# Performance work log

Hardware: AMD Instinct MI355X
Metric: run time of the kernel (lower is better)

Reference implementation:

```python
import jax, jax.numpy as jnp
import numpy as np

EMBED = 1024
HEADS = 16
HEAD_DIM = EMBED // HEADS


def setup_inputs() -> dict:
    key = jax.random.key(0)
    ks = jax.random.split(key, 11)
    B, S, D = 2, 2048, EMBED
    scale = 1.0 / np.sqrt(D)
    inp = {
        "q": jax.random.normal(ks[0], (B, S, D), jnp.float32),
        "k": jax.random.normal(ks[1], (B, S, D), jnp.float32),
        "v": jax.random.normal(ks[2], (B, S, D), jnp.float32),
        "Wq": jax.random.normal(ks[3], (D, D), jnp.float32) * scale,
        "bq": jnp.zeros((D,), jnp.float32),
        "Wk": jax.random.normal(ks[4], (D, D), jnp.float32) * scale,
        "bk": jnp.zeros((D,), jnp.float32),
        "Wv": jax.random.normal(ks[5], (D, D), jnp.float32) * scale,
        "bv": jnp.zeros((D,), jnp.float32),
        "Wo": jax.random.normal(ks[6], (D, D), jnp.float32) * scale,
        "bo": jnp.zeros((D,), jnp.float32),
    }
    return inp


def _split_heads(x):
    b, n, c = x.shape
    return x.reshape(b, n, HEADS, c // HEADS).transpose(0, 2, 1, 3)  # [b,h,n,dh]


def reference(q, k, v, Wq, bq, Wk, bk, Wv, bv, Wo, bo):
    qh = _split_heads(q @ Wq + bq)
    kh = _split_heads(k @ Wk + bk)
    vh = _split_heads(v @ Wv + bv)
    scale = 1.0 / jnp.sqrt(jnp.asarray(HEAD_DIM, qh.dtype))
    att = jnp.einsum("bhqd,bhkd->bhqk", qh, kh) * scale
    att = jax.nn.softmax(att, axis=-1)
    out = jnp.einsum("bhqk,bhkd->bhqd", att, vh)
    b, h, n, dh = out.shape
    out = out.transpose(0, 2, 1, 3).reshape(b, n, h * dh)
    return out @ Wo + bo
```

## Files before the change

kernel.cpp:

```cpp
#include <hip/hip_runtime.h>
#include <hip/hip_bf16.h>
#include <stdint.h>

typedef unsigned short u16;
typedef __bf16 bf16x8 __attribute__((ext_vector_type(8)));
typedef float f32x4 __attribute__((ext_vector_type(4)));
typedef float f32x16 __attribute__((ext_vector_type(16)));
typedef unsigned int u32x4 __attribute__((ext_vector_type(4)));
typedef unsigned int u32x2 __attribute__((ext_vector_type(2)));

#define S_LEN 2048
#define DMODEL 1024
#define NHEAD 16
#define DHEAD 64
#define MROWS 4096
#define EXP2SCALE 0.180336880112f

__device__ __forceinline__ u16 f2b(float f) {
  __hip_bfloat16 h = __float2bfloat16(f);
  union { __hip_bfloat16 h; u16 u; } c;
  c.h = h;
  return c.u;
}
__device__ __forceinline__ unsigned int pk2(float lo, float hi) {
  return (unsigned int)f2b(lo) | ((unsigned int)f2b(hi) << 16);
}
__device__ __forceinline__ unsigned int cvtpk(float a, float b) {
  unsigned int r;
  asm("v_cvt_pk_bf16_f32 %0, %1, %2" : "=v"(r) : "v"(a), "v"(b));
  return r;
}
__device__ __forceinline__ void plswap(unsigned int &a, unsigned int &b) {
  auto r = __builtin_amdgcn_permlane32_swap((int)a, (int)b, false, false);
  a = (unsigned int)r[0];
  b = (unsigned int)r[1];
}

__device__ __forceinline__ void gload16(const void* g, void* l) {
  __builtin_amdgcn_global_load_lds(
      (const __attribute__((address_space(1))) unsigned int*)(uintptr_t)g,
      (__attribute__((address_space(3))) unsigned int*)(uintptr_t)l,
      16, 0, 0);
}

__global__ __launch_bounds__(256) void prep(
    const float* __restrict__ q, const float* __restrict__ k, const float* __restrict__ v,
    const float* __restrict__ Wq, const float* __restrict__ Wk,
    const float* __restrict__ Wv, const float* __restrict__ Wo,
    u16* __restrict__ Qx, u16* __restrict__ Kx, u16* __restrict__ Vx,
    u16* __restrict__ Wqt, u16* __restrict__ Wkt,
    u16* __restrict__ Wvt, u16* __restrict__ Wot) {
  __shared__ u16 tile[64][65];
  const int z = blockIdx.z;
  const int tid = threadIdx.x;
  if (z < 3) {
    const float* src = (z == 0) ? q : (z == 1) ? k : v;
    u16* dst = (z == 0) ? Qx : (z == 1) ? Kx : Vx;
    const size_t i8 = ((size_t)blockIdx.x * 256 + tid) * 8;
    float4 a = *(const float4*)(src + i8);
    float4 b = *(const float4*)(src + i8 + 4);
    u16 o[8];
    o[0] = f2b(a.x); o[1] = f2b(a.y); o[2] = f2b(a.z); o[3] = f2b(a.w);
    o[4] = f2b(b.x); o[5] = f2b(b.y); o[6] = f2b(b.z); o[7] = f2b(b.w);
    *(u32x4*)(dst + i8) = *(const u32x4*)o;
    return;
  }
  if (blockIdx.x >= 256) return;
  const int zz = z - 3;
  const float* W = (zz == 0) ? Wq : (zz == 1) ? Wk : (zz == 2) ? Wv : Wo;
  u16* Wt = (zz == 0) ? Wqt : (zz == 1) ? Wkt : (zz == 2) ? Wvt : Wot;
  const int n0 = (blockIdx.x & 15) * 64, k0 = (blockIdx.x >> 4) * 64;
#pragma unroll
  for (int j = 0; j < 16; j++) {
    int idx = j * 256 + tid;
    int r = idx >> 6, c = idx & 63;
    tile[r][c] = f2b(W[(size_t)(k0 + r) * DMODEL + n0 + c]);
  }
  __syncthreads();
#pragma unroll
  for (int j = 0; j < 16; j++) {
    int idx = j * 256 + tid;
    int r = idx >> 6, c = idx & 63;
    Wt[(size_t)(n0 + r) * DMODEL + k0 + c] = tile[c][r];
  }
}

template <int MODE, int BM>
__device__ __forceinline__ void gemm_body(const u16* __restrict__ A,
                                          const u16* __restrict__ Bt,
                                          const float* __restrict__ bias,
                                          void* __restrict__ Cv,
                                          u16* __restrict__ As,
                                          u16* __restrict__ Bs) {
  constexpr int K = DMODEL;
  constexpr int MB = MROWS / BM;
  constexpr int TA = BM / 32;
  constexpr int NI = BM / 32;
  const int tid = threadIdx.x;
  const int wave = tid >> 6, lane = tid & 63;
  const int quad = lane >> 4, l15 = lane & 15;
  const int wr = wave >> 1, wc = wave & 1;
  const int lid = blockIdx.y * 8 + blockIdx.x;
  const int sw = (lid & 7) * MB + (lid >> 3);
  const int bcol = sw & 7, brow = sw >> 3;

  f32x4 acc[NI][4] = {};

  for (int k0 = 0; k0 < K; k0 += 64) {
    __syncthreads();
#pragma unroll
    for (int t = 0; t < TA; t++) {
      const int slot = t * 256 + wave * 64 + lane;
      const int row = slot >> 3;
      const int cgc = ((slot & 7) ^ (row & 7)) << 3;
      const int ldsb = (t * 256 + wave * 64) * 8;
      gload16(A + (size_t)(brow * BM + row) * K + k0 + cgc, As + ldsb);
    }
#pragma unroll
    for (int t = 0; t < 4; t++) {
      const int slot = t * 256 + wave * 64 + lane;
      const int row = slot >> 3;
      const int cgc = ((slot & 7) ^ (row & 7)) << 3;
      const int ldsb = (t * 256 + wave * 64) * 8;
      gload16(Bt + (size_t)(bcol * 128 + row) * K + k0 + cgc, Bs + ldsb);
    }
    __syncthreads();

#pragma unroll
    for (int kk = 0; kk < 2; kk++) {
      bf16x8 af[NI], bfm[4];
#pragma unroll
      for (int i = 0; i < NI; i++)
        af[i] = *(const bf16x8*)(As + (wr * (BM / 2) + i * 16 + l15) * 64 +
                                 ((((kk << 2) + quad) ^ (l15 & 7)) << 3));
#pragma unroll
      for (int j = 0; j < 4; j++)
        bfm[j] = *(const bf16x8*)(Bs + (wc * 64 + j * 16 + l15) * 64 +
                                  ((((kk << 2) + quad) ^ (l15 & 7)) << 3));
#pragma unroll
      for (int i = 0; i < NI; i++)
#pragma unroll
        for (int j = 0; j < 4; j++)
          acc[i][j] = __builtin_amdgcn_mfma_f32_16x16x32_bf16(af[i], bfm[j], acc[i][j], 0, 0, 0);
    }
  }

#pragma unroll
  for (int i = 0; i < NI; i++)
#pragma unroll
    for (int j = 0; j < 4; j++) {
      const int col = bcol * 128 + wc * 64 + j * 16 + l15;
      const float bv = bias[col];
      if (MODE == 2) {
        const int srow = brow * BM + wr * (BM / 2) + i * 16 + quad * 4;
        const int bb = srow >> 11, s = srow & (S_LEN - 1);
        u32x2 pd;
        pd.x = pk2(acc[i][j][0] + bv, acc[i][j][1] + bv);
        pd.y = pk2(acc[i][j][2] + bv, acc[i][j][3] + bv);
        *(u32x2*)((u16*)Cv + ((size_t)(bb * 1024 + col)) * S_LEN + s) = pd;
      } else {
#pragma unroll
        for (int r = 0; r < 4; r++) {
          const int row = brow * BM + wr * (BM / 2) + i * 16 + quad * 4 + r;
          if (MODE == 1)
            ((float*)Cv)[(size_t)row * DMODEL + col] = acc[i][j][r] + bv;
          else if (MODE == 3)
            ((u16*)Cv)[(size_t)row * DMODEL + col] = f2b((acc[i][j][r] + bv) * EXP2SCALE);
          else
            ((u16*)Cv)[(size_t)row * DMODEL + col] = f2b(acc[i][j][r] + bv);
        }
      }
    }
}

__global__ __launch_bounds__(256, 4) void gemm_qkv(
    const u16* __restrict__ Qx, const u16* __restrict__ Kx, const u16* __restrict__ Vx,
    const u16* __restrict__ Wqt, const u16* __restrict__ Wkt, const u16* __restrict__ Wvt,
    const float* __restrict__ bq, const float* __restrict__ bk, const float* __restrict__ bv,
    u16* __restrict__ Qp, u16* __restrict__ Kp, u16* __restrict__ Vt) {
  __shared__ u16 As[128 * 64];
  __shared__ u16 Bs[128 * 64];
  const int z = blockIdx.z;
  if (z == 2) {
    gemm_body<2, 128>(Vx, Wvt, bv, Vt, As, Bs);
  } else if (z == 0) {
    gemm_body<3, 128>(Qx, Wqt, bq, Qp, As, Bs);
  } else {
    gemm_body<0, 128>(Kx, Wkt, bk, Kp, As, Bs);
  }
}

__global__ __launch_bounds__(256, 4) void gemm_out(
    const u16* __restrict__ A, const u16* __restrict__ Bt,
    const float* __restrict__ bias, float* __restrict__ C) {
  __shared__ u16 As[64 * 64];
  __shared__ u16 Bs[128 * 64];
  gemm_body<1, 64>(A, Bt, bias, C, As, Bs);
}

#define TILE_COMPUTE(ksb, vsb)                                                     \
  do {                                                                             \
    f32x16 sA = {}, sB = {};                                                       \
    __builtin_amdgcn_s_setprio(1);                                                 \
    _Pragma("unroll") for (int c = 0; c < 4; c++) {                                \
      bf16x8 ka0 = *(const bf16x8*)((ksb) + off[c]);                               \
      bf16x8 ka1 = *(const bf16x8*)((ksb) + off[c] + 2048);                        \
      sA = __builtin_amdgcn_mfma_f32_32x32x16_bf16(ka0, qf[c], sA, 0, 0, 0);       \
      sB = __builtin_amdgcn_mfma_f32_32x32x16_bf16(ka1, qf[c], sB, 0, 0, 0);       \
    }                                                                              \
    __builtin_amdgcn_s_setprio(0);                                                 \
    bf16x8 pf[4];                                                                  \
    _Pragma("unroll") for (int kb = 0; kb < 2; kb++) {                             \
      const f32x16 s = kb ? sB : sA;                                               \
      unsigned int cc[8];                                                          \
      _Pragma("unroll") for (int m = 0; m < 8; m++)                                \
        cc[m] = cvtpk(__builtin_amdgcn_exp2f(s[2 * m]),                            \
                      __builtin_amdgcn_exp2f(s[2 * m + 1]));                       \
      plswap(cc[0], cc[2]);                                                        \
      plswap(cc[1], cc[3]);                                                        \
      plswap(cc[4], cc[6]);                                                        \
      plswap(cc[5], cc[7]);                                                        \
      union { unsigned int u[4]; bf16x8 v; } f0, f1;                               \
      f0.u[0] = cc[0]; f0.u[1] = cc[1]; f0.u[2] = cc[2]; f0.u[3] = cc[3];          \
      f1.u[0] = cc[4]; f1.u[1] = cc[5]; f1.u[2] = cc[6]; f1.u[3] = cc[7];          \
      pf[2 * kb] = f0.v; pf[2 * kb + 1] = f1.v;                                    \
    }                                                                              \
    __builtin_amdgcn_s_setprio(1);                                                 \
    _Pragma("unroll") for (int g = 0; g < 4; g++) {                                \
      bf16x8 v0 = *(const bf16x8*)((vsb) + off[g]);                                \
      bf16x8 v1 = *(const bf16x8*)((vsb) + off[g] + 2048);                         \
      lacc  = __builtin_amdgcn_mfma_f32_32x32x16_bf16(pf[g], ones, lacc, 0, 0, 0); \
      oacc0 = __builtin_amdgcn_mfma_f32_32x32x16_bf16(pf[g], v0, oacc0, 0, 0, 0);  \
      oacc1 = __builtin_amdgcn_mfma_f32_32x32x16_bf16(pf[g], v1, oacc1, 0, 0, 0);  \
    }                                                                              \
    __builtin_amdgcn_s_setprio(0);                                                 \
  } while (0)

#define ISSUE(buf, kt)                                                            \
  do {                                                                            \
    if (wave < 4) {                                                               \
      const u16* g = srcK + (size_t)(kt) * 64 * DMODEL;                           \
      _Pragma("unroll") for (int j = 0; j < 4; j++)                               \
        gload16(g + (size_t)j * 8 * DMODEL, dst0 + (buf) * 4096 + j * 512);       \
    } else {                                                                      \
      const u16* g = srcV + (kt) * 64;                                            \
      _Pragma("unroll") for (int j = 0; j < 4; j++)                               \
        gload16(g + (size_t)j * 8 * S_LEN, dst0 + (buf) * 4096 + j * 512);        \
    }                                                                             \
  } while (0)

__global__ __launch_bounds__(512, 4) void attn(const u16* __restrict__ Qp,
                                               const u16* __restrict__ Kp,
                                               const u16* __restrict__ Vt,
                                               u16* __restrict__ Op) {
  __shared__ u16 LB[32768];

  const int tid = threadIdx.x;
  const int wave = tid >> 6, lane = tid & 63;
  const int row31 = lane & 31, hl = lane >> 5;
  const int qg = wave & 3, kh = wave >> 2;

  const int id = blockIdx.x + (blockIdx.y << 4) + (blockIdx.z << 8);
  const int sw = ((id & 7) << 6) + (id >> 3);
  const int qt = sw & 15, h = (sw >> 4) & 15, b = sw >> 8;
  const int s0 = qt * 128;

  const size_t baseK = ((size_t)(b * S_LEN)) * DMODEL + h * DHEAD;
  const size_t baseV = ((size_t)((b * NHEAD + h) * DHEAD)) * S_LEN;

  const int sub = wave & 1, khd = (wave >> 1) & 1;
  const int rl = lane >> 3, cl = lane & 7;
  const int cg8 = (cl ^ rl) << 3;
  const u16* srcK = Kp + baseK + (size_t)(khd * 1024 + sub * 32 + rl) * DMODEL + cg8;
  const u16* srcV = Vt + baseV + (size_t)(sub * 32 + rl) * S_LEN + khd * 1024 + cg8;
  u16* dst0 = LB + (wave >= 4 ? 16384 : 0) + khd * 8192 + (sub * 32) * 64;

  const u16* kcb = LB + kh * 8192;
  const u16* vcb = LB + 16384 + kh * 8192;

  int off[4];
#pragma unroll
  for (int c = 0; c < 4; c++)
    off[c] = row31 * 64 + ((((c << 1) + hl) ^ (row31 & 7)) << 3);

  bf16x8 ones;
  {
    union { u16 a[8]; bf16x8 v; } c;
#pragma unroll
    for (int j = 0; j < 8; j++) c.a[j] = 0x3F80;
    ones = c.v;
  }

  bf16x8 qf[4];
#pragma unroll
  for (int c = 0; c < 4; c++)
    qf[c] = *(const bf16x8*)(Qp +
        ((size_t)(b * S_LEN + s0 + qg * 32 + row31)) * DMODEL +
        h * DHEAD + c * 16 + hl * 8);

  f32x16 oacc0 = {}, oacc1 = {};
  f32x16 lacc = {};

  ISSUE(0, 0);

#pragma unroll 1
  for (int kt = 0; kt < 16; kt += 2) {
    __syncthreads();
    ISSUE(1, kt + 1);
    TILE_COMPUTE(kcb, vcb);
    __syncthreads();
    if (kt + 2 < 16) ISSUE(0, kt + 2);
    TILE_COMPUTE(kcb + 4096, vcb + 4096);
  }

  __syncthreads();
  float* M = ((float*)LB) + qg * 3072;
  if (kh == 1) {
#pragma unroll
    for (int r = 0; r < 16; r++) {
      M[r * 64 + lane]        = oacc0[r];
      M[1024 + r * 64 + lane] = oacc1[r];
      M[2048 + r * 64 + lane] = lacc[r];
    }
  }
  __syncthreads();
  if (kh == 0) {
#pragma unroll
    for (int r = 0; r < 16; r++) {
      const float o0 = oacc0[r] + M[r * 64 + lane];
      const float o1 = oacc1[r] + M[1024 + r * 64 + lane];
      const float ls = lacc[r] + M[2048 + r * 64 + lane];
      const float inv = 1.0f / ls;
      const int qrow = (r & 3) + 8 * (r >> 2) + 4 * hl;
      const size_t rb = ((size_t)(b * S_LEN + s0 + qg * 32 + qrow)) * DMODEL + h * DHEAD;
      Op[rb + row31]      = f2b(o0 * inv);
      Op[rb + 32 + row31] = f2b(o1 * inv);
    }
  }
}

extern "C" void kernel_launch(void* const* d_in, const int* in_sizes, int n_in,
                              void* d_out, int out_size, void* d_ws, size_t ws_size,
                              hipStream_t stream) {
  const float* q  = (const float*)d_in[0];
  const float* k  = (const float*)d_in[1];
  const float* v  = (const float*)d_in[2];
  const float* Wq = (const float*)d_in[3];
  const float* bq = (const float*)d_in[4];
  const float* Wk = (const float*)d_in[5];
  const float* bk = (const float*)d_in[6];
  const float* Wv = (const float*)d_in[7];
  const float* bv = (const float*)d_in[8];
  const float* Wo = (const float*)d_in[9];
  const float* bo = (const float*)d_in[10];

  char* w = (char*)d_ws;
  const size_t WSZ = (size_t)DMODEL * DMODEL * 2;
  const size_t XSZ = (size_t)MROWS * DMODEL * 2;
  u16* Wqt = (u16*)(w);
  u16* Wkt = (u16*)(w + WSZ);
  u16* Wvt = (u16*)(w + 2 * WSZ);
  u16* Wot = (u16*)(w + 3 * WSZ);
  u16* Qx  = (u16*)(w + 4 * WSZ);
  u16* Kx  = (u16*)(w + 4 * WSZ + XSZ);
  u16* Vx  = (u16*)(w + 4 * WSZ + 2 * XSZ);
  u16* Qp  = (u16*)(w + 4 * WSZ + 3 * XSZ);
  u16* Kp  = (u16*)(w + 4 * WSZ + 4 * XSZ);
  u16* Vt  = (u16*)(w + 4 * WSZ + 5 * XSZ);
  u16* Op  = (u16*)(w + 4 * WSZ + 6 * XSZ);

  prep<<<dim3(2048, 1, 7), 256, 0, stream>>>(q, k, v, Wq, Wk, Wv, Wo,
                                             Qx, Kx, Vx, Wqt, Wkt, Wvt, Wot);
  gemm_qkv<<<dim3(8, 32, 3), 256, 0, stream>>>(Qx, Kx, Vx, Wqt, Wkt, Wvt,
                                               bq, bk, bv, Qp, Kp, Vt);
  attn<<<dim3(16, 16, 2), 512, 0, stream>>>(Qp, Kp, Vt, Op);
  gemm_out<<<dim3(8, 64, 1), 256, 0, stream>>>(Op, Wot, bo, (float*)d_out);
}
```

Before: 209.5 us.

## Triple-buffer GEMM K-loop with async global-to-LDS prefetch two stages ahead

Replaces the single-buffered 64-wide K loop in the shared GEMM body with a 3-stage ring of 32-wide K slices. Each slice is loaded into LDS asynchronously two iterations ahead, and a counted vmcnt wait plus a single barrier per step replaces the two syncthreads. The LDS swizzle changes to fit 32-element rows, and MFMA issue is bracketed with setprio. This is meant to hide global-load latency behind the MFMA work. In exchange the barrier count doubles because K steps are halved, and gemm_qkv's launch bound drops to 3 blocks per SM, which may lower occupancy.

```diff
diff --git a/kernel.cpp b/kernel.cpp
--- a/kernel.cpp
+++ b/kernel.cpp
@@ -93,9 +93,13 @@
                                           u16* __restrict__ As,
                                           u16* __restrict__ Bs) {
   constexpr int K = DMODEL;
+  constexpr int NS = K / 32;
   constexpr int MB = MROWS / BM;
-  constexpr int TA = BM / 32;
+  constexpr int TA = BM / 64;
   constexpr int NI = BM / 32;
+  constexpr int ASZ = BM * 32;
+  constexpr int BSZ = 128 * 32;
+  constexpr int VW = TA + 2;
   const int tid = threadIdx.x;
   const int wave = tid >> 6, lane = tid & 63;
   const int quad = lane >> 4, l15 = lane & 15;
@@ -106,43 +110,57 @@
 
   f32x4 acc[NI][4] = {};
 
-  for (int k0 = 0; k0 < K; k0 += 64) {
-    __syncthreads();
+  auto issue = [&](int b, int s) {
 #pragma unroll
     for (int t = 0; t < TA; t++) {
       const int slot = t * 256 + wave * 64 + lane;
-      const int row = slot >> 3;
-      const int cgc = ((slot & 7) ^ (row & 7)) << 3;
-      const int ldsb = (t * 256 + wave * 64) * 8;
-      gload16(A + (size_t)(brow * BM + row) * K + k0 + cgc, As + ldsb);
-    }
-#pragma unroll
-    for (int t = 0; t < 4; t++) {
+      const int row = slot >> 2;
+      const int cgc = ((slot & 3) ^ ((row >> 1) & 3)) << 3;
+      gload16(A + (size_t)(brow * BM + row) * K + s * 32 + cgc,
+              As + b * ASZ + (t * 256 + wave * 64) * 8);
+    }
+#pragma unroll
+    for (int t = 0; t < 2; t++) {
       const int slot = t * 256 + wave * 64 + lane;
-      const int row = slot >> 3;
-      const int cgc = ((slot & 7) ^ (row & 7)) << 3;
-      const int ldsb = (t * 256 + wave * 64) * 8;
-      gload16(Bt + (size_t)(bcol * 128 + row) * K + k0 + cgc, Bs + ldsb);
-    }
-    __syncthreads();
-
-#pragma unroll
-    for (int kk = 0; kk < 2; kk++) {
-      bf16x8 af[NI], bfm[4];
-#pragma unroll
-      for (int i = 0; i < NI; i++)
-        af[i] = *(const bf16x8*)(As + (wr * (BM / 2) + i * 16 + l15) * 64 +
-                                 ((((kk << 2) + quad) ^ (l15 & 7)) << 3));
+      const int row = slot >> 2;
+      const int cgc = ((slot & 3) ^ ((row >> 1) & 3)) << 3;
+      gload16(Bt + (size_t)(bcol * 128 + row) * K + s * 32 + cgc,
+              Bs + b * BSZ + (t * 256 + wave * 64) * 8);
+    }
+  };
+
+  issue(0, 0);
+  issue(1, 1);
+
+#pragma unroll 1
+  for (int k = 0; k < NS; ++k) {
+    asm volatile("s_waitcnt lgkmcnt(0)" ::: "memory");
+    if (k == NS - 1)
+      asm volatile("s_waitcnt vmcnt(0)" ::: "memory");
+    else
+      asm volatile("s_waitcnt vmcnt(%0)" :: "i"(VW) : "memory");
+    __builtin_amdgcn_s_barrier();
+    __builtin_amdgcn_sched_barrier(0);
+    if (k + 2 < NS) issue((k + 2) % 3, k + 2);
+
+    const u16* Ab = As + (k % 3) * ASZ;
+    const u16* Bb = Bs + (k % 3) * BSZ;
+    bf16x8 af[NI], bfm[4];
+#pragma unroll
+    for (int i = 0; i < NI; i++)
+      af[i] = *(const bf16x8*)(Ab + (wr * (BM / 2) + i * 16 + l15) * 32 +
+                               ((quad ^ ((l15 >> 1) & 3)) << 3));
+#pragma unroll
+    for (int j = 0; j < 4; j++)
+      bfm[j] = *(const bf16x8*)(Bb + (wc * 64 + j * 16 + l15) * 32 +
+                                ((quad ^ ((l15 >> 1) & 3)) << 3));
+    __builtin_amdgcn_s_setprio(1);
+#pragma unroll
+    for (int i = 0; i < NI; i++)
 #pragma unroll
       for (int j = 0; j < 4; j++)
-        bfm[j] = *(const bf16x8*)(Bs + (wc * 64 + j * 16 + l15) * 64 +
-                                  ((((kk << 2) + quad) ^ (l15 & 7)) << 3));
-#pragma unroll
-      for (int i = 0; i < NI; i++)
-#pragma unroll
-        for (int j = 0; j < 4; j++)
-          acc[i][j] = __builtin_amdgcn_mfma_f32_16x16x32_bf16(af[i], bfm[j], acc[i][j], 0, 0, 0);
-    }
+        acc[i][j] = __builtin_amdgcn_mfma_f32_16x16x32_bf16(af[i], bfm[j], acc[i][j], 0, 0, 0);
+    __builtin_amdgcn_s_setprio(0);
   }
 
 #pragma unroll
@@ -173,13 +191,13 @@
     }
 }
 
-__global__ __launch_bounds__(256, 4) void gemm_qkv(
+__global__ __launch_bounds__(256, 3) void gemm_qkv(
     const u16* __restrict__ Qx, const u16* __restrict__ Kx, const u16* __restrict__ Vx,
     const u16* __restrict__ Wqt, const u16* __restrict__ Wkt, const u16* __restrict__ Wvt,
     const float* __restrict__ bq, const float* __restrict__ bk, const float* __restrict__ bv,
     u16* __restrict__ Qp, u16* __restrict__ Kp, u16* __restrict__ Vt) {
-  __shared__ u16 As[128 * 64];
-  __shared__ u16 Bs[128 * 64];
+  __shared__ u16 As[3 * 128 * 32];
+  __shared__ u16 Bs[3 * 128 * 32];
   const int z = blockIdx.z;
   if (z == 2) {
     gemm_body<2, 128>(Vx, Wvt, bv, Vt, As, Bs);
@@ -193,8 +211,8 @@
 __global__ __launch_bounds__(256, 4) void gemm_out(
     const u16* __restrict__ A, const u16* __restrict__ Bt,
     const float* __restrict__ bias, float* __restrict__ C) {
-  __shared__ u16 As[64 * 64];
-  __shared__ u16 Bs[128 * 64];
+  __shared__ u16 As[3 * 64 * 32];
+  __shared__ u16 Bs[3 * 128 * 32];
   gemm_body<1, 64>(A, Bt, bias, C, As, Bs);
 }
 
```

Result: no change. 211.8 us (+1.1%).

## Load GEMM operands directly from global into registers with software double-buffering

Applied to the files above, without the earlier changes.

The projection GEMMs stop staging A and B tiles through LDS. Each lane now loads its MFMA fragments straight from global memory into two register buffers and alternates loads with MFMA batches, which removes the per-k-step barriers. The transposed V output is staged through a swizzled LDS tile so global stores become 16-byte row-contiguous writes, and the QKV launch bound drops from 4 to 3 to leave room for the extra registers. Without LDS reuse, every wave refetches its operands from L2/global, which raises memory traffic and may expose load latency.

```diff
diff --git a/kernel.cpp b/kernel.cpp
--- a/kernel.cpp
+++ b/kernel.cpp
@@ -90,12 +90,11 @@
                                           const u16* __restrict__ Bt,
                                           const float* __restrict__ bias,
                                           void* __restrict__ Cv,
-                                          u16* __restrict__ As,
-                                          u16* __restrict__ Bs) {
+                                          u16* __restrict__ Ct) {
   constexpr int K = DMODEL;
   constexpr int MB = MROWS / BM;
-  constexpr int TA = BM / 32;
   constexpr int NI = BM / 32;
+  constexpr int NJ = 4;
   const int tid = threadIdx.x;
   const int wave = tid >> 6, lane = tid & 63;
   const int quad = lane >> 4, l15 = lane & 15;
@@ -104,98 +103,113 @@
   const int sw = (lid & 7) * MB + (lid >> 3);
   const int bcol = sw & 7, brow = sw >> 3;
 
-  f32x4 acc[NI][4] = {};
-
-  for (int k0 = 0; k0 < K; k0 += 64) {
-    __syncthreads();
-#pragma unroll
-    for (int t = 0; t < TA; t++) {
-      const int slot = t * 256 + wave * 64 + lane;
-      const int row = slot >> 3;
-      const int cgc = ((slot & 7) ^ (row & 7)) << 3;
-      const int ldsb = (t * 256 + wave * 64) * 8;
-      gload16(A + (size_t)(brow * BM + row) * K + k0 + cgc, As + ldsb);
-    }
-#pragma unroll
-    for (int t = 0; t < 4; t++) {
-      const int slot = t * 256 + wave * 64 + lane;
-      const int row = slot >> 3;
-      const int cgc = ((slot & 7) ^ (row & 7)) << 3;
-      const int ldsb = (t * 256 + wave * 64) * 8;
-      gload16(Bt + (size_t)(bcol * 128 + row) * K + k0 + cgc, Bs + ldsb);
-    }
-    __syncthreads();
-
-#pragma unroll
-    for (int kk = 0; kk < 2; kk++) {
-      bf16x8 af[NI], bfm[4];
-#pragma unroll
-      for (int i = 0; i < NI; i++)
-        af[i] = *(const bf16x8*)(As + (wr * (BM / 2) + i * 16 + l15) * 64 +
-                                 ((((kk << 2) + quad) ^ (l15 & 7)) << 3));
-#pragma unroll
-      for (int j = 0; j < 4; j++)
-        bfm[j] = *(const bf16x8*)(Bs + (wc * 64 + j * 16 + l15) * 64 +
-                                  ((((kk << 2) + quad) ^ (l15 & 7)) << 3));
-#pragma unroll
-      for (int i = 0; i < NI; i++)
-#pragma unroll
-        for (int j = 0; j < 4; j++)
-          acc[i][j] = __builtin_amdgcn_mfma_f32_16x16x32_bf16(af[i], bfm[j], acc[i][j], 0, 0, 0);
-    }
-  }
-
+  const u16* pA[NI];
+  const u16* pB[NJ];
 #pragma unroll
   for (int i = 0; i < NI; i++)
-#pragma unroll
-    for (int j = 0; j < 4; j++) {
-      const int col = bcol * 128 + wc * 64 + j * 16 + l15;
-      const float bv = bias[col];
-      if (MODE == 2) {
-        const int srow = brow * BM + wr * (BM / 2) + i * 16 + quad * 4;
-        const int bb = srow >> 11, s = srow & (S_LEN - 1);
+    pA[i] = A + (size_t)(brow * BM + wr * (BM / 2) + i * 16 + l15) * K + quad * 8;
+#pragma unroll
+  for (int j = 0; j < NJ; j++)
+    pB[j] = Bt + (size_t)(bcol * 128 + wc * 64 + j * 16 + l15) * K + quad * 8;
+
+#define LOADAB(av, bv, kk)                                    \
+  do {                                                        \
+    _Pragma("unroll") for (int i = 0; i < NI; i++)            \
+      av[i] = *(const bf16x8*)(pA[i] + (kk) * 32);            \
+    _Pragma("unroll") for (int j = 0; j < NJ; j++)            \
+      bv[j] = *(const bf16x8*)(pB[j] + (kk) * 32);            \
+  } while (0)
+
+#define MFMAS(av, bv)                                                          \
+  do {                                                                         \
+    __builtin_amdgcn_s_setprio(1);                                             \
+    _Pragma("unroll") for (int i = 0; i < NI; i++)                             \
+      _Pragma("unroll") for (int j = 0; j < NJ; j++)                           \
+        acc[i][j] = __builtin_amdgcn_mfma_f32_16x16x32_bf16(av[i], bv[j],      \
+                                                            acc[i][j], 0, 0, 0); \
+    __builtin_amdgcn_s_setprio(0);                                             \
+  } while (0)
+
+  f32x4 acc[NI][NJ] = {};
+  bf16x8 a0[NI], b0[NJ], a1[NI], b1[NJ];
+
+  LOADAB(a0, b0, 0);
+#pragma unroll 1
+  for (int k = 0; k < 32; k += 2) {
+    LOADAB(a1, b1, k + 1);
+    MFMAS(a0, b0);
+    if (k + 2 < 32) LOADAB(a0, b0, k + 2);
+    MFMAS(a1, b1);
+  }
+#undef LOADAB
+#undef MFMAS
+
+  if (MODE == 2) {
+#pragma unroll
+    for (int i = 0; i < NI; i++)
+#pragma unroll
+      for (int j = 0; j < NJ; j++) {
+        const int n = wc * 64 + j * 16 + l15;
+        const float bv = bias[bcol * 128 + n];
+        const int m = wr * (BM / 2) + i * 16 + quad * 4;
+        const int mc = m >> 3;
         u32x2 pd;
         pd.x = pk2(acc[i][j][0] + bv, acc[i][j][1] + bv);
         pd.y = pk2(acc[i][j][2] + bv, acc[i][j][3] + bv);
-        *(u32x2*)((u16*)Cv + ((size_t)(bb * 1024 + col)) * S_LEN + s) = pd;
-      } else {
-#pragma unroll
-        for (int r = 0; r < 4; r++) {
-          const int row = brow * BM + wr * (BM / 2) + i * 16 + quad * 4 + r;
-          if (MODE == 1)
-            ((float*)Cv)[(size_t)row * DMODEL + col] = acc[i][j][r] + bv;
-          else if (MODE == 3)
-            ((u16*)Cv)[(size_t)row * DMODEL + col] = f2b((acc[i][j][r] + bv) * EXP2SCALE);
-          else
-            ((u16*)Cv)[(size_t)row * DMODEL + col] = f2b(acc[i][j][r] + bv);
-        }
+        *(u32x2*)(Ct + n * BM + ((mc ^ (n & (BM / 8 - 1))) << 3) + (m & 7)) = pd;
+      }
+    __syncthreads();
+    const int c0 = bcol * 128, sr0 = brow * BM;
+    const int bb = sr0 >> 11, sbase = sr0 & (S_LEN - 1);
+#pragma unroll
+    for (int p = 0; p < 128 * BM / 8 / 256; p++) {
+      const int idx = p * 256 + tid;
+      const int cl = idx / (BM / 8), sc = idx & (BM / 8 - 1);
+      *(u32x4*)((u16*)Cv + ((size_t)(bb * 1024 + c0 + cl)) * S_LEN + sbase + sc * 8) =
+          *(const u32x4*)(Ct + cl * BM + ((sc ^ (cl & (BM / 8 - 1))) << 3));
+    }
+    return;
+  }
+
+#pragma unroll
+  for (int i = 0; i < NI; i++)
+#pragma unroll
+    for (int j = 0; j < NJ; j++) {
+      const int col = bcol * 128 + wc * 64 + j * 16 + l15;
+      const float bv = bias[col];
+#pragma unroll
+      for (int r = 0; r < 4; r++) {
+        const int row = brow * BM + wr * (BM / 2) + i * 16 + quad * 4 + r;
+        if (MODE == 1)
+          ((float*)Cv)[(size_t)row * DMODEL + col] = acc[i][j][r] + bv;
+        else if (MODE == 3)
+          ((u16*)Cv)[(size_t)row * DMODEL + col] = f2b((acc[i][j][r] + bv) * EXP2SCALE);
+        else
+          ((u16*)Cv)[(size_t)row * DMODEL + col] = f2b(acc[i][j][r] + bv);
       }
     }
 }
 
-__global__ __launch_bounds__(256, 4) void gemm_qkv(
+__global__ __launch_bounds__(256, 3) void gemm_qkv(
     const u16* __restrict__ Qx, const u16* __restrict__ Kx, const u16* __restrict__ Vx,
     const u16* __restrict__ Wqt, const u16* __restrict__ Wkt, const u16* __restrict__ Wvt,
     const float* __restrict__ bq, const float* __restrict__ bk, const float* __restrict__ bv,
     u16* __restrict__ Qp, u16* __restrict__ Kp, u16* __restrict__ Vt) {
-  __shared__ u16 As[128 * 64];
-  __shared__ u16 Bs[128 * 64];
+  __shared__ u16 Ct[128 * 128];
   const int z = blockIdx.z;
   if (z == 2) {
-    gemm_body<2, 128>(Vx, Wvt, bv, Vt, As, Bs);
+    gemm_body<2, 128>(Vx, Wvt, bv, Vt, Ct);
   } else if (z == 0) {
-    gemm_body<3, 128>(Qx, Wqt, bq, Qp, As, Bs);
+    gemm_body<3, 128>(Qx, Wqt, bq, Qp, Ct);
   } else {
-    gemm_body<0, 128>(Kx, Wkt, bk, Kp, As, Bs);
+    gemm_body<0, 128>(Kx, Wkt, bk, Kp, Ct);
   }
 }
 
 __global__ __launch_bounds__(256, 4) void gemm_out(
     const u16* __restrict__ A, const u16* __restrict__ Bt,
     const float* __restrict__ bias, float* __restrict__ C) {
-  __shared__ u16 As[64 * 64];
-  __shared__ u16 Bs[128 * 64];
-  gemm_body<1, 64>(A, Bt, bias, C, As, Bs);
+  gemm_body<1, 64>(A, Bt, bias, C, nullptr);
 }
 
 #define TILE_COMPUTE(ksb, vsb)                                                     \
```

Result: slower. 293.8 us (+40.3%).
